# Kernel tuning notes

Measured on AMD Instinct MI355X. Metric: run time of the kernel, lower is better.

Reference implementation:

```python
import jax, jax.numpy as jnp
import numpy as np

N = 50000   # nodes
E = 600000  # edges (avg degree 12)
D = 128     # node feature dim (input == hidden so residual applies)
R = 7       # num_relation
G = 32      # num graphs in the batch
L = 3       # layers
W_SCALE = 0.02


def setup_inputs() -> dict:
    key = jax.random.key(0)
    ks = jax.random.split(key, 5 + 2 * L)
    inp = {
        "x": jax.random.normal(ks[0], (N, D), jnp.float32),
        "node_in": jax.random.randint(ks[1], (E,), 0, N),
        "node_out": jax.random.randint(ks[2], (E,), 0, N),
        "relation": jax.random.randint(ks[3], (E,), 0, R),
        "edge_weight": jnp.ones((E,), jnp.float32),
        "node2graph": jnp.sort(jax.random.randint(ks[4], (N,), 0, G)),
        "num_node": N,
        "num_graphs": G,
    }
    for i in range(L):
        inp[f"sl_w{i}"] = jax.random.normal(ks[5 + 2 * i], (D, D), jnp.float32) * W_SCALE
        inp[f"sl_b{i}"] = jnp.zeros((D,), jnp.float32)
        inp[f"lin_w{i}"] = jax.random.normal(ks[6 + 2 * i], (R * D, D), jnp.float32) * W_SCALE
        inp[f"lin_b{i}"] = jnp.zeros((D,), jnp.float32)
    return inp


def _gearnet(x, edge_weight, params, node_in, node_out, relation, node2graph,
             num_node, num_graphs):
    # relation-keyed scatter index: node_out * R + relation
    idx = node_out * R + relation  # [E]
    h = x
    for (sl_w, sl_b, lin_w, lin_b) in params:
        din = h.shape[1]
        msg = h[node_in] * edge_weight[:, None]                           # [E, din] gather
        agg = jax.ops.segment_sum(msg, idx, num_segments=num_node * R)    # [N*R, din] scatter_add
        upd = agg.reshape(num_node, R * din)                              # [N, R*din]
        out = jax.nn.relu(upd @ lin_w + lin_b + h @ sl_w + sl_b)          # combine: linear + self_loop, relu
        h = out + h                                                        # short_cut residual (shapes match)
    node_feature = h
    graph_feature = jax.ops.segment_sum(node_feature, node2graph, num_segments=num_graphs)  # SumReadout
    return graph_feature, node_feature


def reference(x, node_in, node_out, relation, edge_weight, node2graph,
              sl_w0, sl_b0, lin_w0, lin_b0,
              sl_w1, sl_b1, lin_w1, lin_b1,
              sl_w2, sl_b2, lin_w2, lin_b2,
              num_node, num_graphs):
    params = [(sl_w0, sl_b0, lin_w0, lin_b0),
              (sl_w1, sl_b1, lin_w1, lin_b1),
              (sl_w2, sl_b2, lin_w2, lin_b2)]
    return _gearnet(x, edge_weight, params, node_in, node_out, relation,
                    node2graph, num_node, num_graphs)
```

## Files before the change

### kernel.cpp

```cpp
#include <hip/hip_runtime.h>
#include <hip/hip_bf16.h>

#define NN 50000
#define EE 600000
#define DD 128
#define RR 7
#define SS 8
#define GG 32
#define NSEG (NN * RR)
#define NB1 ((NSEG + 1023) / 1024)

typedef float f32x4 __attribute__((ext_vector_type(4)));
typedef float f32x2 __attribute__((ext_vector_type(2)));
typedef short short8 __attribute__((ext_vector_type(8)));
typedef unsigned short u16x8 __attribute__((ext_vector_type(8)));

static __device__ __forceinline__ unsigned short f2bf(float f) {
    union { float f; unsigned u; } v; v.f = f;
    unsigned r = v.u + 0x7fff + ((v.u >> 16) & 1);
    return (unsigned short)(r >> 16);
}
static __device__ __forceinline__ float bf2f(unsigned short u) {
    union { unsigned u; float f; } v; v.u = ((unsigned)u) << 16;
    return v.f;
}

__global__ void prep_w2(const float* __restrict__ lin_w, const float* __restrict__ sl_w,
                        const float* __restrict__ lin_b, const float* __restrict__ sl_b,
                        unsigned short* __restrict__ Wt2, float* __restrict__ bias) {
    int idx = blockIdx.x * 256 + threadIdx.x;
    if (idx < DD) bias[idx] = lin_b[idx] + sl_b[idx];
    if (idx >= 1024 * DD) return;
    int j = idx >> 7;
    int k = idx & 127;
    int slot = j >> 7, dout = j & 127;
    float w = (slot < 7) ? lin_w[(slot * DD + k) * DD + dout] : sl_w[k * DD + dout];
    Wt2[(size_t)j * DD + k] = f2bf(w);
}

__global__ void zero_ints(int* __restrict__ p, int n) {
    int i = blockIdx.x * 256 + threadIdx.x;
    if (i < n) p[i] = 0;
}

__global__ void hist(const int* __restrict__ node_out, const int* __restrict__ rel,
                     int* __restrict__ counts) {
    int e = blockIdx.x * 256 + threadIdx.x;
    if (e >= EE) return;
    atomicAdd(&counts[node_out[e] * RR + rel[e]], 1);
}

__global__ __launch_bounds__(256) void scan1(const int* __restrict__ counts,
                                             int* __restrict__ start, int* __restrict__ bsum) {
    __shared__ int s[256];
    int tid = threadIdx.x;
    int base = blockIdx.x * 1024 + tid * 4;
    int v[4], sum = 0;
    #pragma unroll
    for (int j = 0; j < 4; ++j) {
        v[j] = (base + j < NSEG) ? counts[base + j] : 0;
        sum += v[j];
    }
    s[tid] = sum; __syncthreads();
    for (int off = 1; off < 256; off <<= 1) {
        int t = (tid >= off) ? s[tid - off] : 0;
        __syncthreads();
        s[tid] += t;
        __syncthreads();
    }
    int run = s[tid] - sum;
    if (tid == 255) bsum[blockIdx.x] = s[255];
    #pragma unroll
    for (int j = 0; j < 4; ++j) {
        if (base + j < NSEG) { start[base + j] = run; run += v[j]; }
    }
}

__global__ __launch_bounds__(512) void scan2(int* __restrict__ bsum) {
    __shared__ int s[512];
    int tid = threadIdx.x;
    int v = (tid < NB1) ? bsum[tid] : 0;
    s[tid] = v; __syncthreads();
    for (int off = 1; off < 512; off <<= 1) {
        int t = (tid >= off) ? s[tid - off] : 0;
        __syncthreads();
        s[tid] += t;
        __syncthreads();
    }
    if (tid < NB1) bsum[tid] = s[tid] - v;
}

__global__ void scan3(const int* __restrict__ start, const int* __restrict__ bsum,
                      const int* __restrict__ counts, int2* __restrict__ segd) {
    int i = blockIdx.x * 256 + threadIdx.x;
    if (i < NSEG) segd[i] = make_int2(start[i] + bsum[i >> 10], counts[i]);
}

__global__ void fill(const int* __restrict__ node_in, const int* __restrict__ node_out,
                     const int* __restrict__ rel, const float* __restrict__ ew,
                     const int2* __restrict__ segd, int* __restrict__ cursor,
                     int2* __restrict__ edges) {
    int e = blockIdx.x * 256 + threadIdx.x;
    if (e >= EE) return;
    int seg = node_out[e] * RR + rel[e];
    int pos = segd[seg].x + atomicAdd(&cursor[seg], 1);
    edges[pos] = make_int2((rel[e] << 16) | node_in[e], __float_as_int(ew[e]));
}

__global__ void init_hb(const float* __restrict__ x, unsigned short* __restrict__ hb) {
    int t = blockIdx.x * 256 + threadIdx.x;
    if (t >= NN * 32) return;
    f32x4 v = ((const f32x4*)x)[t];
    unsigned long long pack = (unsigned long long)f2bf(v.x)
                            | ((unsigned long long)f2bf(v.y) << 16)
                            | ((unsigned long long)f2bf(v.z) << 32)
                            | ((unsigned long long)f2bf(v.w) << 48);
    ((unsigned long long*)hb)[t] = pack;
}

__global__ __launch_bounds__(256) void gemm_p(
        const unsigned short* __restrict__ hb,
        const unsigned short* __restrict__ Wt2,
        unsigned short* __restrict__ P) {
    int tid = threadIdx.x;
    int wid = tid >> 6, lane = tid & 63;
    int wr = wid >> 1, wc = wid & 1;
    int lm = lane & 15, lg = lane >> 4;
    int bm0 = (blockIdx.x >> 2) * 128;
    int cb0 = (blockIdx.x & 3) * 2;

    short8 af[4][4];
    #pragma unroll
    for (int mi = 0; mi < 4; ++mi) {
        int gr = bm0 + wr * 64 + mi * 16 + lm;
        #pragma unroll
        for (int ks = 0; ks < 4; ++ks) {
            short8 t = {};
            if (gr < NN) t = *(const short8*)(hb + (size_t)gr * DD + ks * 32 + lg * 8);
            af[mi][ks] = t;
        }
    }
    #pragma unroll
    for (int cc = 0; cc < 2; ++cc) {
        int cb = cb0 + cc;
        f32x4 acc[4][4] = {};
        #pragma unroll
        for (int ks = 0; ks < 4; ++ks) {
            short8 bfr[4];
            #pragma unroll
            for (int ni = 0; ni < 4; ++ni)
                bfr[ni] = *(const short8*)(Wt2 + (size_t)(cb * 128 + wc * 64 + ni * 16 + lm) * DD
                                           + ks * 32 + lg * 8);
            #pragma unroll
            for (int mi = 0; mi < 4; ++mi)
                #pragma unroll
                for (int ni = 0; ni < 4; ++ni)
                    acc[mi][ni] = __builtin_amdgcn_mfma_f32_16x16x32_bf16(af[mi][ks], bfr[ni], acc[mi][ni], 0, 0, 0);
        }
        #pragma unroll
        for (int mi = 0; mi < 4; ++mi) {
            #pragma unroll
            for (int v = 0; v < 4; ++v) {
                int gm = bm0 + wr * 64 + mi * 16 + lg * 4 + v;
                if (gm >= NN) continue;
                #pragma unroll
                for (int ni = 0; ni < 4; ++ni) {
                    int j = cb * 128 + wc * 64 + ni * 16 + lm;
                    P[(size_t)gm * 1024 + j] = f2bf(acc[mi][ni][v]);
                }
            }
        }
    }
}

#define PROW(r) (const unsigned*)(P + (size_t)((((r).x & 0xFFFF) << 3) | ((r).x >> 16)) * DD + lane * 2)
__global__ __launch_bounds__(256) void gather_p(
        const unsigned short* __restrict__ P,
        const int2* __restrict__ segd,
        const int2* __restrict__ edges,
        const float* __restrict__ bias,
        const float* __restrict__ hprev,
        float* __restrict__ hout,
        unsigned short* __restrict__ hb_next,
        int write_next) {
    int tid = threadIdx.x;
    int wv = tid >> 6, lane = tid & 63;
    int node = blockIdx.x * 4 + wv;
    int st = segd[node * RR].x;
    int2 s6 = segd[node * RR + 6];
    int end = s6.x + s6.y;

    float ax = 0.f, ay = 0.f;
    int2 r0 = edges[st];
    int2 r1 = edges[st + 1];
    int2 r2 = edges[st + 2];
    int2 r3 = edges[st + 3];
    int2 r4 = edges[st + 4];
    unsigned hv0 = *PROW(r0);
    unsigned hv1 = *PROW(r1);
    unsigned hv2 = *PROW(r2);
    unsigned hv3 = *PROW(r3);
    for (int i = st; i < end; ++i) {
        int2 r5 = edges[i + 5];
        unsigned hv4 = *PROW(r4);
        float w = __int_as_float(r0.y);
        ax += bf2f((unsigned short)(hv0 & 0xFFFF)) * w;
        ay += bf2f((unsigned short)(hv0 >> 16)) * w;
        r0 = r1; r1 = r2; r2 = r3; r3 = r4; r4 = r5;
        hv0 = hv1; hv1 = hv2; hv2 = hv3; hv3 = hv4;
    }
    unsigned hs = *(const unsigned*)(P + ((size_t)node * 8 + 7) * DD + lane * 2);
    float bx = bias[lane * 2], by = bias[lane * 2 + 1];
    f32x2 hp = ((const f32x2*)hprev)[(size_t)node * 64 + lane];
    float vx = fmaxf(ax + bf2f((unsigned short)(hs & 0xFFFF)) + bx, 0.f) + hp.x;
    float vy = fmaxf(ay + bf2f((unsigned short)(hs >> 16)) + by, 0.f) + hp.y;
    ((f32x2*)hout)[(size_t)node * 64 + lane] = (f32x2){vx, vy};
    if (write_next)
        ((unsigned*)hb_next)[(size_t)node * 64 + lane] =
            (unsigned)f2bf(vx) | ((unsigned)f2bf(vy) << 16);
}

__global__ void zero_gf(float* gf) {
    int t = blockIdx.x * 256 + threadIdx.x;
    if (t < GG * DD) gf[t] = 0.f;
}

__global__ __launch_bounds__(256) void readout(const float* __restrict__ h,
                                               const int* __restrict__ n2g,
                                               float* __restrict__ gf) {
    int c0 = blockIdx.x * 128;
    int rg = threadIdx.x >> 5, d4 = threadIdx.x & 31;
    f32x4 acc = {0.f, 0.f, 0.f, 0.f};
    int cur = -1;
    #pragma unroll 4
    for (int it = 0; it < 16; ++it) {
        int row = c0 + it * 8 + rg;
        if (row >= NN) break;
        int g = n2g[row];
        if (g != cur) {
            if (cur >= 0) {
                atomicAdd(&gf[cur * DD + d4 * 4 + 0], acc.x);
                atomicAdd(&gf[cur * DD + d4 * 4 + 1], acc.y);
                atomicAdd(&gf[cur * DD + d4 * 4 + 2], acc.z);
                atomicAdd(&gf[cur * DD + d4 * 4 + 3], acc.w);
            }
            cur = g;
            acc = (f32x4){0.f, 0.f, 0.f, 0.f};
        }
        acc += ((const f32x4*)h)[(size_t)row * 32 + d4];
    }
    if (cur >= 0) {
        atomicAdd(&gf[cur * DD + d4 * 4 + 0], acc.x);
        atomicAdd(&gf[cur * DD + d4 * 4 + 1], acc.y);
        atomicAdd(&gf[cur * DD + d4 * 4 + 2], acc.z);
        atomicAdd(&gf[cur * DD + d4 * 4 + 3], acc.w);
    }
}

extern "C" void kernel_launch(void* const* d_in, const int* in_sizes, int n_in,
                              void* d_out, int out_size, void* d_ws, size_t ws_size,
                              hipStream_t stream) {
    const float* x      = (const float*)d_in[0];
    const int* node_in  = (const int*)d_in[1];
    const int* node_out = (const int*)d_in[2];
    const int* relation = (const int*)d_in[3];
    const float* ew     = (const float*)d_in[4];
    const int* n2g      = (const int*)d_in[5];
    const float* sl_w[3]  = {(const float*)d_in[8],  (const float*)d_in[12], (const float*)d_in[16]};
    const float* sl_b[3]  = {(const float*)d_in[9],  (const float*)d_in[13], (const float*)d_in[17]};
    const float* lin_w[3] = {(const float*)d_in[10], (const float*)d_in[14], (const float*)d_in[18]};
    const float* lin_b[3] = {(const float*)d_in[11], (const float*)d_in[15], (const float*)d_in[19]};

    float* out = (float*)d_out;
    float* gf = out;
    float* nf = out + GG * DD;

    char* ws = (char*)d_ws;
    size_t off = 0;
    unsigned short* P  = (unsigned short*)(ws + off); off += (size_t)NN * 1024 * 2;
    unsigned short* hb0 = (unsigned short*)(ws + off); off += (size_t)NN * DD * 2;
    unsigned short* hb1 = (unsigned short*)(ws + off); off += (size_t)NN * DD * 2;
    float* hA   = (float*)(ws + off);            off += (size_t)NN * DD * 4;
    unsigned short* Wt2 = (unsigned short*)(ws + off); off += (size_t)3 * 1024 * DD * 2;
    float* bias = (float*)(ws + off);            off += 3 * DD * 4;
    int* counts = (int*)(ws + off);              off += (size_t)NSEG * 4;
    int* cursor = (int*)(ws + off);              off += (size_t)NSEG * 4;
    int* start  = (int*)(ws + off);              off += (size_t)NSEG * 4;
    int2* segd  = (int2*)(ws + off);             off += (size_t)NSEG * 8;
    int* bsum   = (int*)(ws + off);              off += 512 * 4;
    int2* edges = (int2*)(ws + off);             off += (size_t)(EE + 8) * 8;

    for (int l = 0; l < 3; ++l)
        prep_w2<<<512, 256, 0, stream>>>(lin_w[l], sl_w[l], lin_b[l], sl_b[l],
                                         Wt2 + (size_t)l * 1024 * DD, bias + l * DD);

    zero_ints<<<(2 * NSEG + 255) / 256, 256, 0, stream>>>(counts, 2 * NSEG);
    zero_ints<<<1, 64, 0, stream>>>((int*)(edges + EE), 16);
    hist<<<(EE + 255) / 256, 256, 0, stream>>>(node_out, relation, counts);
    scan1<<<NB1, 256, 0, stream>>>(counts, start, bsum);
    scan2<<<1, 512, 0, stream>>>(bsum);
    scan3<<<(NSEG + 255) / 256, 256, 0, stream>>>(start, bsum, counts, segd);
    fill<<<(EE + 255) / 256, 256, 0, stream>>>(node_in, node_out, relation, ew,
                                               segd, cursor, edges);
    init_hb<<<(NN * 32) / 256, 256, 0, stream>>>(x, hb0);

    const float* hcur = x;
    float* houts[3] = { nf, hA, nf };
    unsigned short* hbs[2] = { hb0, hb1 };
    for (int l = 0; l < 3; ++l) {
        gemm_p<<<((NN + 127) / 128) * 4, 256, 0, stream>>>(
            hbs[l & 1], Wt2 + (size_t)l * 1024 * DD, P);
        gather_p<<<NN / 4, 256, 0, stream>>>(
            P, segd, edges, bias + l * DD, hcur, houts[l],
            hbs[(l + 1) & 1], l < 2 ? 1 : 0);
        hcur = houts[l];
    }
    zero_gf<<<(GG * DD + 255) / 256, 256, 0, stream>>>(gf);
    readout<<<(NN + 127) / 128, 256, 0, stream>>>(nf, n2g, gf);
}
```

Before: 422.4 us.

## Stage GEMM output through LDS for coalesced 16-byte stores and retile blocks

```diff
diff --git a/kernel.cpp b/kernel.cpp
--- a/kernel.cpp
+++ b/kernel.cpp
@@ -118,21 +118,22 @@
     ((unsigned long long*)hb)[t] = pack;
 }
 
+#define LSTR 136
 __global__ __launch_bounds__(256) void gemm_p(
         const unsigned short* __restrict__ hb,
         const unsigned short* __restrict__ Wt2,
         unsigned short* __restrict__ P) {
+    __shared__ unsigned short sOut[64 * LSTR];
     int tid = threadIdx.x;
     int wid = tid >> 6, lane = tid & 63;
     int wr = wid >> 1, wc = wid & 1;
     int lm = lane & 15, lg = lane >> 4;
-    int bm0 = (blockIdx.x >> 2) * 128;
-    int cb0 = (blockIdx.x & 3) * 2;
-
-    short8 af[4][4];
+    int bm0 = blockIdx.x * 64;
+
+    short8 af[2][4];
     #pragma unroll
-    for (int mi = 0; mi < 4; ++mi) {
-        int gr = bm0 + wr * 64 + mi * 16 + lm;
+    for (int mi = 0; mi < 2; ++mi) {
+        int gr = bm0 + wr * 32 + mi * 16 + lm;
         #pragma unroll
         for (int ks = 0; ks < 4; ++ks) {
             short8 t = {};
@@ -140,10 +141,8 @@
             af[mi][ks] = t;
         }
     }
-    #pragma unroll
-    for (int cc = 0; cc < 2; ++cc) {
-        int cb = cb0 + cc;
-        f32x4 acc[4][4] = {};
+    for (int cb = 0; cb < 8; ++cb) {
+        f32x4 acc[2][4] = {};
         #pragma unroll
         for (int ks = 0; ks < 4; ++ks) {
             short8 bfr[4];
@@ -152,23 +151,31 @@
                 bfr[ni] = *(const short8*)(Wt2 + (size_t)(cb * 128 + wc * 64 + ni * 16 + lm) * DD
                                            + ks * 32 + lg * 8);
             #pragma unroll
-            for (int mi = 0; mi < 4; ++mi)
+            for (int mi = 0; mi < 2; ++mi)
                 #pragma unroll
                 for (int ni = 0; ni < 4; ++ni)
                     acc[mi][ni] = __builtin_amdgcn_mfma_f32_16x16x32_bf16(af[mi][ks], bfr[ni], acc[mi][ni], 0, 0, 0);
         }
+        __syncthreads();
         #pragma unroll
-        for (int mi = 0; mi < 4; ++mi) {
+        for (int mi = 0; mi < 2; ++mi)
             #pragma unroll
-            for (int v = 0; v < 4; ++v) {
-                int gm = bm0 + wr * 64 + mi * 16 + lg * 4 + v;
-                if (gm >= NN) continue;
+            for (int ni = 0; ni < 4; ++ni)
                 #pragma unroll
-                for (int ni = 0; ni < 4; ++ni) {
-                    int j = cb * 128 + wc * 64 + ni * 16 + lm;
-                    P[(size_t)gm * 1024 + j] = f2bf(acc[mi][ni][v]);
+                for (int v = 0; v < 4; ++v) {
+                    int row = wr * 32 + mi * 16 + lg * 4 + v;
+                    int col = wc * 64 + ni * 16 + lm;
+                    sOut[row * LSTR + col] = f2bf(acc[mi][ni][v]);
                 }
-            }
+        __syncthreads();
+        #pragma unroll
+        for (int it = 0; it < 4; ++it) {
+            int q = it * 256 + tid;
+            int row = q >> 4, c = q & 15;
+            int gm = bm0 + row;
+            if (gm < NN)
+                *(u16x8*)(P + (size_t)gm * 1024 + cb * 128 + c * 8) =
+                    *(const u16x8*)(sOut + row * LSTR + c * 8);
         }
     }
 }
@@ -308,7 +315,7 @@
     float* houts[3] = { nf, hA, nf };
     unsigned short* hbs[2] = { hb0, hb1 };
     for (int l = 0; l < 3; ++l) {
-        gemm_p<<<((NN + 127) / 128) * 4, 256, 0, stream>>>(
+        gemm_p<<<(NN + 63) / 64, 256, 0, stream>>>(
             hbs[l & 1], Wt2 + (size_t)l * 1024 * DD, P);
         gather_p<<<NN / 4, 256, 0, stream>>>(
             P, segd, edges, bias + l * DD, hcur, houts[l],
```

Result: slower. 468.6 us (+10.9%).
